# Kernel tuning notes

Measured on AMD Instinct MI355X. Metric: run time of the kernel, lower is better.

Reference implementation:

```python
import jax, jax.numpy as jnp
import numpy as np

B, N, C0, N0 = 2, 4096, 128, 10242
IN_CH = 19  # 16 class-label + 3 xyz channels of `original`
EPS = 1e-5


def setup_inputs() -> dict:
    key = jax.random.key(0)
    ks = jax.random.split(key, 8)
    original = jax.random.normal(ks[0], (B, IN_CH, N), dtype=jnp.float32)
    projected = jax.random.normal(ks[1], (B, C0, N0), dtype=jnp.float32)
    vertex = jax.random.normal(ks[2], (N0, 3), dtype=jnp.float32)
    near_idx = jax.random.randint(ks[3], (N0, 6), 1, N0)  # low=1 so threshold > 0
    W0 = jax.random.normal(ks[4], (128, IN_CH + C0), dtype=jnp.float32) * 0.02
    W1 = jax.random.normal(ks[5], (128, 128), dtype=jnp.float32) * 0.02
    W2 = jax.random.normal(ks[6], (128, 128), dtype=jnp.float32) * 0.02
    z = jnp.zeros((128,), jnp.float32)
    o = jnp.ones((128,), jnp.float32)
    return {
        'original': original, 'projected': projected, 'vertex': vertex,
        'near_idx': near_idx,
        'W0': W0, 'b0': z, 'g0': o, 'be0': z,
        'W1': W1, 'b1': z, 'g1': o, 'be1': z,
        'W2': W2, 'b2': z, 'g2': o, 'be2': z,
    }


def _sf_to_pc(proj_f, vertex, near_idx, xyz):
    # proj_f: [B, N0, C0] features per mesh vertex; xyz: [B, N, 3]
    r = jnp.sqrt(jnp.sum(vertex[0] ** 2))  # sphere radius of fractal mesh
    # spherical projection of xyz onto sphere radius r (same direction)
    pxyz = xyz * (r / jnp.linalg.norm(xyz, axis=-1, keepdims=True))  # [B,N,3]
    # threshold = dist(vertex[0], vertex[near_idx[0,0]]); compare squared dists
    t2 = jnp.sum((vertex[0] - vertex[near_idx[0, 0]]) ** 2)
    # squared distances via GEMM: |p|^2 = r^2 (on sphere)
    v2 = jnp.sum(vertex ** 2, axis=-1)  # [N0]
    d2 = r * r + v2[None, None, :] - 2.0 * jnp.einsum('bnd,md->bnm', pxyz, vertex)
    mask = d2 <= t2                              # [B,N,N0]
    has = jnp.any(mask, axis=-1)                 # [B,N]
    first = jnp.argmax(mask, axis=-1)            # first matching vertex (early-exit semantics)
    feat = jnp.take_along_axis(proj_f, first[..., None], axis=1)  # [B,N,C0]
    return jnp.where(has[..., None], feat, 0.0)


def _conv_bn_relu(x, W, b, g, be):
    # x: [B,N,Cin]; 1x1 Conv1d == per-point linear; BN over (B,N) per channel (train mode)
    y = jnp.einsum('bnc,oc->bno', x, W) + b
    mean = jnp.mean(y, axis=(0, 1))
    var = jnp.var(y, axis=(0, 1))
    y = g * (y - mean) * jax.lax.rsqrt(var + EPS) + be
    return jax.nn.relu(y)


def reference(original, projected, vertex, near_idx,
              W0, b0, g0, be0, W1, b1, g1, be1, W2, b2, g2, be2):
    orig = jnp.transpose(original, (0, 2, 1))    # [B,N,19]
    proj_f = jnp.transpose(projected, (0, 2, 1))  # [B,N0,C0]
    xyz = orig[:, :, :3]
    feat = _sf_to_pc(proj_f, vertex, near_idx, xyz)      # [B,N,C0]
    x = jnp.concatenate([orig, feat], axis=-1)           # [B,N,19+C0]
    x = _conv_bn_relu(x, W0, b0, g0, be0)
    x = _conv_bn_relu(x, W1, b1, g1, be1)
    x = _conv_bn_relu(x, W2, b2, g2, be2)
    return jnp.transpose(x, (0, 2, 1))  # [B,128,N]
```

## Files before the change

kernel.cpp:

```cpp
#include <hip/hip_runtime.h>

#define NPTS 4096
#define N0V  10242
#define EPSV 1e-5f
#define SLOTS 16

typedef unsigned short ushortT;
typedef __attribute__((ext_vector_type(8))) short short8;
typedef __attribute__((ext_vector_type(4))) float f32x4;

__device__ __forceinline__ float fmul(float a,float b){return __fmul_rn(a,b);}
__device__ __forceinline__ float fadd(float a,float b){return __fadd_rn(a,b);}
__device__ __forceinline__ float fsub(float a,float b){return __fsub_rn(a,b);}

__device__ __forceinline__ ushortT f2bf(float x){
  unsigned u = __float_as_uint(x);
  u = (u + 0x7fffu + ((u>>16)&1u)) >> 16;
  return (ushortT)u;
}

template<int NS>
__device__ __forceinline__ void tile_mm(const ushortT* xa, const ushortT* wt, int wstr,
    int li, int hi, int rt, int colg, f32x4& acc)
{
  acc = (f32x4){0.f,0.f,0.f,0.f};
  const ushortT* wbp = wt + colg*wstr + hi*8;
  const ushortT* xap = xa + (rt*16 + li)*168 + hi*8;
  #pragma unroll
  for (int s=0;s<NS;s++){
    short8 bb = *(const short8*)(wbp + s*32);
    short8 a0 = *(const short8*)(xap + s*32);
    acc = __builtin_amdgcn_mfma_f32_16x16x32_bf16(a0, bb, acc, 0,0,0);
  }
}

__device__ __forceinline__ void tile_partials(const f32x4& acc, float* __restrict__ slotL,
                                              int blk, int lane, int colg)
{
  float s1=0.f, s2=0.f;
  #pragma unroll
  for (int r=0;r<4;r++){ s1 += acc[r]; s2 = fmaf(acc[r],acc[r],s2); }
  s1 += __shfl_xor(s1,16); s1 += __shfl_xor(s1,32);
  s2 += __shfl_xor(s2,16); s2 += __shfl_xor(s2,32);
  if (lane < 16){
    float* sl = slotL + (blk & (SLOTS-1))*256;
    atomicAdd(&sl[colg], s1);
    atomicAdd(&sl[128 + colg], s2);
  }
}

__device__ __forceinline__ void slot_stats(const float* __restrict__ slotL,
    const float* __restrict__ g, const float* __restrict__ be,
    float* red2, float* stS, float* stB, int t)
{
  if (t < 256){
    float v = 0.f;
    #pragma unroll
    for (int s=0;s<SLOTS;s++) v += slotL[s*256 + t];
    red2[t] = v;
  }
  __syncthreads();
  if (t < 128){
    float S = red2[t], Q = red2[128 + t];
    float mean = S * (1.0f/8192.0f);
    float var  = Q * (1.0f/8192.0f) - mean*mean;
    float inv  = 1.0f / __fsqrt_rn(var + EPSV);
    float sc = g[t]*inv;
    stS[t] = sc;
    stB[t] = be[t] - mean*sc;
  }
  __syncthreads();
}

__global__ __launch_bounds__(1024) void k_l0(
    const float* __restrict__ orig, const float* __restrict__ proj,
    const float* __restrict__ vertex, const int* __restrict__ nidx,
    const float* __restrict__ W0, const float* __restrict__ b0,
    float* __restrict__ slot0, float* __restrict__ y0)
{
  __shared__ __align__(16) ushortT wt[128*168];
  __shared__ __align__(16) ushortT xa[32*168];

  const int t    = threadIdx.x;
  const int blk  = blockIdx.x;
  const int lane = t & 63;
  const int w    = t >> 6;
  const int b    = blk >> 7;
  const int n0   = (blk & 127) * 32;
  const int li   = lane & 15;
  const int hi   = lane >> 4;
  const int rt   = w >> 3;
  const int colg = (w & 7)*16 + li;

  for (int u = t; u < 21504; u += 1024){
    int o = u/168, k = u - o*168;
    wt[u] = f2bf((k < 147) ? W0[o*147 + k] : 0.f);
  }

  {
    float v0x=vertex[0], v0y=vertex[1], v0z=vertex[2];
    float r  = __fsqrt_rn(fadd(fadd(fmul(v0x,v0x),fmul(v0y,v0y)),fmul(v0z,v0z)));
    float rr = fmul(r,r);
    int j0 = nidx[0];
    float ax=vertex[3*j0], ay=vertex[3*j0+1], az=vertex[3*j0+2];
    float dx=fsub(v0x,ax), dy=fsub(v0y,ay), dz=fsub(v0z,az);
    float t2 = fadd(fadd(fmul(dx,dx),fmul(dy,dy)),fmul(dz,dz));

    #pragma unroll
    for (int rr_i=0; rr_i<2; rr_i++){
      const int row = w*2 + rr_i;
      const int n = n0 + row;
      const float* ob = orig + (b*19)*NPTS + n;
      float x=ob[0], y=ob[NPTS], z=ob[2*NPTS];
      float nrm = __fsqrt_rn(fadd(fadd(fmul(x,x),fmul(y,y)),fmul(z,z)));
      float s = __fdiv_rn(r,nrm);
      float px=fmul(x,s), py=fmul(y,s), pz=fmul(z,s);

      int first=0, has=0;
      for (int c0=0; c0<N0V; c0+=256){
        int m0=min(c0+lane,N0V-1), m1=min(c0+lane+64,N0V-1),
            m2=min(c0+lane+128,N0V-1), m3=min(c0+lane+192,N0V-1);
        float a0x=vertex[3*m0],a0y=vertex[3*m0+1],a0z=vertex[3*m0+2];
        float a1x=vertex[3*m1],a1y=vertex[3*m1+1],a1z=vertex[3*m1+2];
        float a2x=vertex[3*m2],a2y=vertex[3*m2+1],a2z=vertex[3*m2+2];
        float a3x=vertex[3*m3],a3y=vertex[3*m3+1],a3z=vertex[3*m3+2];
        float v20=fadd(fadd(fmul(a0x,a0x),fmul(a0y,a0y)),fmul(a0z,a0z));
        float v21=fadd(fadd(fmul(a1x,a1x),fmul(a1y,a1y)),fmul(a1z,a1z));
        float v22=fadd(fadd(fmul(a2x,a2x),fmul(a2y,a2y)),fmul(a2z,a2z));
        float v23=fadd(fadd(fmul(a3x,a3x),fmul(a3y,a3y)),fmul(a3z,a3z));
        float d0=fadd(fadd(fmul(px,a0x),fmul(py,a0y)),fmul(pz,a0z));
        float d1=fadd(fadd(fmul(px,a1x),fmul(py,a1y)),fmul(pz,a1z));
        float d2=fadd(fadd(fmul(px,a2x),fmul(py,a2y)),fmul(pz,a2z));
        float d3=fadd(fadd(fmul(px,a3x),fmul(py,a3y)),fmul(pz,a3z));
        bool h0 = (c0+lane    <N0V) && (fsub(fadd(rr,v20),fmul(2.0f,d0)) <= t2);
        bool h1 = (c0+lane+64 <N0V) && (fsub(fadd(rr,v21),fmul(2.0f,d1)) <= t2);
        bool h2 = (c0+lane+128<N0V) && (fsub(fadd(rr,v22),fmul(2.0f,d2)) <= t2);
        bool h3 = (c0+lane+192<N0V) && (fsub(fadd(rr,v23),fmul(2.0f,d3)) <= t2);
        unsigned long long bal;
        if ((bal=__ballot(h0))){ first=c0     +__builtin_ctzll(bal); has=1; break; }
        if ((bal=__ballot(h1))){ first=c0+ 64+__builtin_ctzll(bal); has=1; break; }
        if ((bal=__ballot(h2))){ first=c0+128+__builtin_ctzll(bal); has=1; break; }
        if ((bal=__ballot(h3))){ first=c0+192+__builtin_ctzll(bal); has=1; break; }
      }

      ushortT* rowp = xa + row*168;
      const float* pb = proj + (long)b*128*N0V;
      #pragma unroll
      for (int k=0;k<3;k++){
        int idx = lane + k*64;
        if (idx < 168){
          float v;
          if (idx < 19)        v = orig[(b*19+idx)*NPTS + n];
          else if (idx < 147)  v = has ? pb[(long)(idx-19)*N0V + first] : 0.0f;
          else                 v = 0.0f;
          rowp[idx] = f2bf(v);
        }
      }
    }
  }
  __syncthreads();

  f32x4 acc;
  tile_mm<5>(xa, wt, 168, li, hi, rt, colg, acc);
  float bo = b0[colg];
  #pragma unroll
  for (int r=0;r<4;r++) acc[r] += bo;
  tile_partials(acc, slot0, blk, lane, colg);
  #pragma unroll
  for (int r=0;r<4;r++)
    y0[(long)(b*4096 + n0 + rt*16 + hi*4 + r)*128 + colg] = acc[r];
}

__global__ __launch_bounds__(1024) void k_lmid(
    const float* __restrict__ yin, const float* __restrict__ slotPrev,
    const float* __restrict__ g, const float* __restrict__ be,
    const float* __restrict__ W, const float* __restrict__ bias,
    float* __restrict__ slotCur, float* __restrict__ yout)
{
  __shared__ __align__(16) ushortT wt[128*136];
  __shared__ __align__(16) ushortT xa[32*168];
  __shared__ float red2[256];
  __shared__ float stS[128];
  __shared__ float stB[128];

  const int t    = threadIdx.x;
  const int blk  = blockIdx.x;
  const int lane = t & 63;
  const int w    = t >> 6;
  const int n0   = blk * 32;
  const int li   = lane & 15;
  const int hi   = lane >> 4;
  const int rt   = w >> 3;
  const int colg = (w & 7)*16 + li;

  for (int u = t; u < 17408; u += 1024){
    int o = u/136, k = u - o*136;
    wt[u] = f2bf((k < 128) ? W[o*128 + k] : 0.f);
  }
  slot_stats(slotPrev, g, be, red2, stS, stB, t);

  for (int i = t; i < 32*168; i += 1024){
    int row = i/168, c = i - row*168;
    float v = 0.f;
    if (c < 128) v = fmaxf(fmaf(yin[(long)(n0+row)*128 + c], stS[c], stB[c]), 0.f);
    xa[i] = f2bf(v);
  }
  __syncthreads();

  f32x4 acc;
  tile_mm<4>(xa, wt, 136, li, hi, rt, colg, acc);
  float bo = bias[colg];
  #pragma unroll
  for (int r=0;r<4;r++) acc[r] += bo;
  tile_partials(acc, slotCur, blk, lane, colg);
  #pragma unroll
  for (int r=0;r<4;r++)
    yout[(long)(n0 + rt*16 + hi*4 + r)*128 + colg] = acc[r];
}

__global__ __launch_bounds__(1024) void k_out(
    const float* __restrict__ yin, const float* __restrict__ slotPrev,
    const float* __restrict__ g, const float* __restrict__ be,
    float* __restrict__ out)
{
  __shared__ float ft[32*132];
  __shared__ float red2[256];
  __shared__ float stS[128];
  __shared__ float stB[128];

  const int t   = threadIdx.x;
  const int blk = blockIdx.x;
  const int b   = blk >> 7;
  const int n0  = (blk & 127) * 32;

  slot_stats(slotPrev, g, be, red2, stS, stB, t);

  for (int i = t; i < 32*128; i += 1024){
    int row = i >> 7, c = i & 127;
    ft[row*132 + c] = fmaxf(fmaf(yin[(long)(b*4096 + n0 + row)*128 + c], stS[c], stB[c]), 0.f);
  }
  __syncthreads();

  float* ob = out + (long)b*128*NPTS + n0;
  {
    int oo = t >> 3, jj = (t & 7) * 4;
    float4 v;
    v.x = ft[(jj  )*132 + oo];
    v.y = ft[(jj+1)*132 + oo];
    v.z = ft[(jj+2)*132 + oo];
    v.w = ft[(jj+3)*132 + oo];
    *(float4*)(ob + (long)oo*NPTS + jj) = v;
  }
}

extern "C" void kernel_launch(void* const* d_in, const int* in_sizes, int n_in,
                              void* d_out, int out_size, void* d_ws, size_t ws_size,
                              hipStream_t stream)
{
  const float* orig   = (const float*)d_in[0];
  const float* proj   = (const float*)d_in[1];
  const float* vertex = (const float*)d_in[2];
  const int*   nidx   = (const int*)d_in[3];
  const float* W0 = (const float*)d_in[4];
  const float* b0 = (const float*)d_in[5];
  const float* g0 = (const float*)d_in[6];
  const float* be0= (const float*)d_in[7];
  const float* W1 = (const float*)d_in[8];
  const float* b1 = (const float*)d_in[9];
  const float* g1 = (const float*)d_in[10];
  const float* be1= (const float*)d_in[11];
  const float* W2 = (const float*)d_in[12];
  const float* b2 = (const float*)d_in[13];
  const float* g2 = (const float*)d_in[14];
  const float* be2= (const float*)d_in[15];
  float* out = (float*)d_out;

  float* ws    = (float*)d_ws;
  float* slot0 = ws;
  float* slot1 = ws + 4096;
  float* slot2 = ws + 8192;
  float* yA    = ws + 12288;
  float* yB    = yA + 8192*128;

  hipMemsetAsync(d_ws, 0, 3*4096*sizeof(float), stream);

  k_l0  <<<256, 1024, 0, stream>>>(orig, proj, vertex, nidx, W0, b0, slot0, yA);
  k_lmid<<<256, 1024, 0, stream>>>(yA, slot0, g0, be0, W1, b1, slot1, yB);
  k_lmid<<<256, 1024, 0, stream>>>(yB, slot1, g1, be1, W2, b2, slot2, yA);
  k_out <<<256, 1024, 0, stream>>>(yA, slot2, g2, be2, out);
}
```

Before: 37.26 us.

## Store intermediate activations in bf16 and fold slot zeroing into first kernel

```diff
diff --git a/kernel.cpp b/kernel.cpp
--- a/kernel.cpp
+++ b/kernel.cpp
@@ -17,6 +17,9 @@
   unsigned u = __float_as_uint(x);
   u = (u + 0x7fffu + ((u>>16)&1u)) >> 16;
   return (ushortT)u;
+}
+__device__ __forceinline__ float bf2f(ushortT u){
+  return __uint_as_float(((unsigned)u) << 16);
 }
 
 template<int NS>
@@ -76,7 +79,8 @@
     const float* __restrict__ orig, const float* __restrict__ proj,
     const float* __restrict__ vertex, const int* __restrict__ nidx,
     const float* __restrict__ W0, const float* __restrict__ b0,
-    float* __restrict__ slot0, float* __restrict__ y0)
+    float* __restrict__ slot0, float* __restrict__ slotZ,
+    ushortT* __restrict__ y0)
 {
   __shared__ __align__(16) ushortT wt[128*168];
   __shared__ __align__(16) ushortT xa[32*168];
@@ -91,6 +95,8 @@
   const int hi   = lane >> 4;
   const int rt   = w >> 3;
   const int colg = (w & 7)*16 + li;
+
+  if (blk < 8) slotZ[blk*1024 + t] = 0.f;
 
   for (int u = t; u < 21504; u += 1024){
     int o = u/168, k = u - o*168;
@@ -168,14 +174,14 @@
   tile_partials(acc, slot0, blk, lane, colg);
   #pragma unroll
   for (int r=0;r<4;r++)
-    y0[(long)(b*4096 + n0 + rt*16 + hi*4 + r)*128 + colg] = acc[r];
+    y0[(long)(b*4096 + n0 + rt*16 + hi*4 + r)*128 + colg] = f2bf(acc[r]);
 }
 
 __global__ __launch_bounds__(1024) void k_lmid(
-    const float* __restrict__ yin, const float* __restrict__ slotPrev,
+    const ushortT* __restrict__ yin, const float* __restrict__ slotPrev,
     const float* __restrict__ g, const float* __restrict__ be,
     const float* __restrict__ W, const float* __restrict__ bias,
-    float* __restrict__ slotCur, float* __restrict__ yout)
+    float* __restrict__ slotCur, ushortT* __restrict__ yout)
 {
   __shared__ __align__(16) ushortT wt[128*136];
   __shared__ __align__(16) ushortT xa[32*168];
@@ -197,13 +203,23 @@
     int o = u/136, k = u - o*136;
     wt[u] = f2bf((k < 128) ? W[o*128 + k] : 0.f);
   }
+  for (int u = t; u < 1280; u += 1024){
+    int row = u/40, c = 128 + (u - row*40);
+    xa[row*168 + c] = 0;
+  }
   slot_stats(slotPrev, g, be, red2, stS, stB, t);
 
-  for (int i = t; i < 32*168; i += 1024){
-    int row = i/168, c = i - row*168;
-    float v = 0.f;
-    if (c < 128) v = fmaxf(fmaf(yin[(long)(n0+row)*128 + c], stS[c], stB[c]), 0.f);
-    xa[i] = f2bf(v);
+  if (t < 512){
+    int row = t >> 4, c0 = (t & 15) * 8;
+    short8 yv = *(const short8*)(yin + (long)(n0+row)*128 + c0);
+    short8 xv;
+    #pragma unroll
+    for (int j=0;j<8;j++){
+      float f = bf2f((ushortT)yv[j]);
+      f = fmaxf(fmaf(f, stS[c0+j], stB[c0+j]), 0.f);
+      xv[j] = (short)f2bf(f);
+    }
+    *(short8*)(xa + row*168 + c0) = xv;
   }
   __syncthreads();
 
@@ -215,11 +231,11 @@
   tile_partials(acc, slotCur, blk, lane, colg);
   #pragma unroll
   for (int r=0;r<4;r++)
-    yout[(long)(n0 + rt*16 + hi*4 + r)*128 + colg] = acc[r];
+    yout[(long)(n0 + rt*16 + hi*4 + r)*128 + colg] = f2bf(acc[r]);
 }
 
 __global__ __launch_bounds__(1024) void k_out(
-    const float* __restrict__ yin, const float* __restrict__ slotPrev,
+    const ushortT* __restrict__ yin, const float* __restrict__ slotPrev,
     const float* __restrict__ g, const float* __restrict__ be,
     float* __restrict__ out)
 {
@@ -235,9 +251,12 @@
 
   slot_stats(slotPrev, g, be, red2, stS, stB, t);
 
-  for (int i = t; i < 32*128; i += 1024){
-    int row = i >> 7, c = i & 127;
-    ft[row*132 + c] = fmaxf(fmaf(yin[(long)(b*4096 + n0 + row)*128 + c], stS[c], stB[c]), 0.f);
+  if (t < 512){
+    int row = t >> 4, c0 = (t & 15) * 8;
+    short8 yv = *(const short8*)(yin + (long)(b*4096 + n0 + row)*128 + c0);
+    #pragma unroll
+    for (int j=0;j<8;j++)
+      ft[row*132 + c0 + j] = fmaxf(fmaf(bf2f((ushortT)yv[j]), stS[c0+j], stB[c0+j]), 0.f);
   }
   __syncthreads();
 
@@ -275,16 +294,16 @@
   const float* be2= (const float*)d_in[15];
   float* out = (float*)d_out;
 
-  float* ws    = (float*)d_ws;
-  float* slot0 = ws;
-  float* slot1 = ws + 4096;
-  float* slot2 = ws + 8192;
-  float* yA    = ws + 12288;
-  float* yB    = yA + 8192*128;
-
-  hipMemsetAsync(d_ws, 0, 3*4096*sizeof(float), stream);
-
-  k_l0  <<<256, 1024, 0, stream>>>(orig, proj, vertex, nidx, W0, b0, slot0, yA);
+  float*   ws    = (float*)d_ws;
+  float*   slot0 = ws;
+  float*   slot1 = ws + 4096;
+  float*   slot2 = ws + 8192;
+  ushortT* yA    = (ushortT*)(ws + 12288);
+  ushortT* yB    = yA + 8192*128;
+
+  hipMemsetAsync(d_ws, 0, 4096*sizeof(float), stream);
+
+  k_l0  <<<256, 1024, 0, stream>>>(orig, proj, vertex, nidx, W0, b0, slot0, slot1, yA);
   k_lmid<<<256, 1024, 0, stream>>>(yA, slot0, g0, be0, W1, b1, slot1, yB);
   k_lmid<<<256, 1024, 0, stream>>>(yB, slot1, g1, be1, W2, b2, slot2, yA);
   k_out <<<256, 1024, 0, stream>>>(yA, slot2, g2, be2, out);
```

Result: faster. 35.44 us (-4.9%).
